# Optimization experiments

Hardware: AMD Instinct MI355X
Metric: run time of the kernel (lower is better)

Reference implementation:

```python
import jax, jax.numpy as jnp
import numpy as np

B, D, C = 4096, 4096, 1024


def setup_inputs() -> dict:
    key = jax.random.key(0)
    kx, kw = jax.random.split(key)
    x = jax.random.normal(kx, (B, D), dtype=jnp.float32)
    # kaiming_normal_ with nonlinearity='relu': std = sqrt(2 / fan_in)
    W = jax.random.normal(kw, (C, D), dtype=jnp.float32) * jnp.sqrt(2.0 / D)
    return {"x": x, "W": W}


def reference(x, W):
    # Original: -( (x[:, :, None] - W.T[None, :, :])**2 ).mean(axis=1)
    d = x.shape[1]
    x_sq = jnp.sum(x * x, axis=1, keepdims=True)        # [B, 1]
    w_sq = jnp.sum(W * W, axis=1)[None, :]              # [1, C]
    cross = jnp.einsum('bd,cd->bc', x, W)               # [B, C] tensor-core GEMM
    return -(x_sq - 2.0 * cross + w_sq) / d
```

## Files before the change

kernel.cpp:

```cpp
#include <hip/hip_runtime.h>
#include <hip/hip_bf16.h>


typedef float f32x4 __attribute__((ext_vector_type(4)));
typedef float f32x2 __attribute__((ext_vector_type(2)));
typedef float f32x16 __attribute__((ext_vector_type(16)));
typedef int i32x4 __attribute__((ext_vector_type(4)));
typedef int i32x8 __attribute__((ext_vector_type(8)));

#define BDIM 4096
#define DDIM 4096
#define CDIM 1024
#define TM 128
#define TN 128
#define BK 64
#define KSPLIT 4
#define NIT ((DDIM / KSPLIT) / BK)
#define SCALE 32.0f
#define INV_SS (1.0f/1024.0f)
#define PSCALE 0.0625f

#define WAITV(N) asm volatile("s_waitcnt vmcnt(" #N ")" ::: "memory")

__global__ __launch_bounds__(256) void cvt_rowsq(
    const float* __restrict__ x, const float* __restrict__ W,
    unsigned char* __restrict__ xb, unsigned char* __restrict__ wb,
    float* __restrict__ xsq, float* __restrict__ wsq)
{
    const int lane = threadIdx.x & 63;
    const int row = blockIdx.x * 4 + (threadIdx.x >> 6);

    const float* src;
    unsigned char* dst;
    float* sq;
    if (row < BDIM) {
        src = x + (size_t)row * DDIM;
        dst = xb + (size_t)row * DDIM;
        sq = xsq + row;
    } else {
        int r = row - BDIM;
        src = W + (size_t)r * DDIM;
        dst = wb + (size_t)r * DDIM;
        sq = wsq + r;
    }

    const float4* s4 = (const float4*)src;
    unsigned int* d4 = (unsigned int*)dst;
    float a = 0.f;
    #pragma unroll
    for (int s = 0; s < DDIM / 4 / 64; ++s) {
        float4 f = s4[lane + 64 * s];
        a += f.x * f.x + f.y * f.y + f.z * f.z + f.w * f.w;
        unsigned int p = 0;
        p = __builtin_amdgcn_cvt_pk_fp8_f32(f.x * SCALE, f.y * SCALE, p, false);
        p = __builtin_amdgcn_cvt_pk_fp8_f32(f.z * SCALE, f.w * SCALE, p, true);
        d4[lane + 64 * s] = p;
    }
    #pragma unroll
    for (int off = 32; off > 0; off >>= 1) a += __shfl_down(a, off);
    if (lane == 0) *sq = a;
}


__device__ __forceinline__ i32x8 cat8(i32x4 lo, i32x4 hi) {
    return __builtin_shufflevector(lo, hi, 0, 1, 2, 3, 4, 5, 6, 7);
}

#define MXMFMA(A, Bv, C)                                                  \
    __builtin_amdgcn_mfma_scale_f32_32x32x64_f8f6f4(                      \
        (A), (Bv), (C), 0, 0, 0, 0x7F7F7F7F, 0, 0x7F7F7F7F)

#define GLOAD16(gp, lp)                                                   \
    __builtin_amdgcn_global_load_lds(                                     \
        (const __attribute__((address_space(1))) void*)(gp),              \
        (__attribute__((address_space(3))) void*)(lp), 16, 0, 0)

__global__ __launch_bounds__(256, 3) void gemm_eucl(
    const unsigned char* __restrict__ xb,
    const unsigned char* __restrict__ wb,
    unsigned int* __restrict__ part)
{
    __shared__ unsigned char sm[3 * 16384];

    const int tid = threadIdx.x;
    const int lane = tid & 63;
    const int w = tid >> 6;
    const int wr = w >> 1;
    const int wc = w & 1;
    const int bm = blockIdx.x * TM;
    const int bn = blockIdx.y * TN;
    const int ks = blockIdx.z * (DDIM / KSPLIT);

    const int srow = w * 32 + (lane >> 2);
    const int schunk = ((lane & 3) ^ ((lane >> 3) & 3)) * 16;
    const unsigned char* gA0 = xb + (size_t)(bm + srow) * DDIM + ks + schunk;
    const unsigned char* gA1 = gA0 + (size_t)16 * DDIM;
    const unsigned char* gB0 = wb + (size_t)(bn + srow) * DDIM + ks + schunk;
    const unsigned char* gB1 = gB0 + (size_t)16 * DDIM;
    unsigned char* lA0 = sm + w * 2048;
    unsigned char* lA1 = lA0 + 1024;
    unsigned char* lB0 = sm + 8192 + w * 2048;
    unsigned char* lB1 = lB0 + 1024;

#define STAGE(q, t)                                                       \
    do {                                                                  \
        GLOAD16(gA0 + (t) * BK, lA0 + (q) * 16384);                       \
        GLOAD16(gA1 + (t) * BK, lA1 + (q) * 16384);                       \
        GLOAD16(gB0 + (t) * BK, lB0 + (q) * 16384);                       \
        GLOAD16(gB1 + (t) * BK, lB1 + (q) * 16384);                       \
    } while (0)

    const int s_rd = ((lane & 31) >> 1) & 3;
    const int c0s = ((lane >> 5) * 2) ^ s_rd;
    const unsigned char* aR0 = sm + (wr * 64 + (lane & 31)) * 64 + c0s * 16;
    const unsigned char* aR1 = sm + (wr * 64 + (lane & 31)) * 64 + (c0s ^ 1) * 16;
    const unsigned char* bR0 = sm + 8192 + (wc * 64 + (lane & 31)) * 64 + c0s * 16;
    const unsigned char* bR1 = sm + 8192 + (wc * 64 + (lane & 31)) * 64 + (c0s ^ 1) * 16;

    f32x16 acc[4] = {};

    STAGE(0, 0);
    STAGE(1, 1);

    #pragma unroll
    for (int t = 0; t < NIT; ++t) {
        const int qo = (t % 3) * 16384;
        if (t + 1 < NIT) WAITV(4);
        else             WAITV(0);
        __builtin_amdgcn_s_barrier();
        if (t + 2 < NIT) STAGE((t + 2) % 3, t + 2);
        i32x8 fb0 = cat8(*(const i32x4*)(bR0 + qo), *(const i32x4*)(bR1 + qo));
        i32x8 fb1 = cat8(*(const i32x4*)(bR0 + qo + 2048),
                         *(const i32x4*)(bR1 + qo + 2048));
        i32x8 fa0 = cat8(*(const i32x4*)(aR0 + qo), *(const i32x4*)(aR1 + qo));
        i32x8 fa1 = cat8(*(const i32x4*)(aR0 + qo + 2048),
                         *(const i32x4*)(aR1 + qo + 2048));
        __builtin_amdgcn_s_setprio(1);
        acc[0] = MXMFMA(fa0, fb0, acc[0]);
        acc[1] = MXMFMA(fa0, fb1, acc[1]);
        acc[2] = MXMFMA(fa1, fb0, acc[2]);
        acc[3] = MXMFMA(fa1, fb1, acc[3]);
        __builtin_amdgcn_s_setprio(0);
    }

    const int bb = blockIdx.x * 8 + blockIdx.y;
    unsigned int* p = part + ((size_t)blockIdx.z * 256 + bb) * 4096;
    #pragma unroll
    for (int f = 0; f < 4; ++f)
        #pragma unroll
        for (int g = 0; g < 4; ++g) {
            unsigned int pk = 0;
            pk = __builtin_amdgcn_cvt_pk_fp8_f32(
                acc[f][g * 4 + 0] * PSCALE, acc[f][g * 4 + 1] * PSCALE, pk, false);
            pk = __builtin_amdgcn_cvt_pk_fp8_f32(
                acc[f][g * 4 + 2] * PSCALE, acc[f][g * 4 + 3] * PSCALE, pk, true);
            p[(f * 4 + g) * 256 + tid] = pk;
        }
#undef STAGE
}

__global__ __launch_bounds__(256) void reduce_out(
    const unsigned int* __restrict__ part, const float* __restrict__ xsq,
    const float* __restrict__ wsq, float* __restrict__ out)
{
    const int bid = blockIdx.x;
    const int bb = bid >> 1;
    const int half = bid & 1;
    const int t = threadIdx.x;
    const int lane = t & 63;
    const int w = t >> 6;
    const int wr = w >> 1, wc = w & 1;
    const int bm = (bb >> 3) * TM, bn = (bb & 7) * TN;
    const size_t sl = (size_t)256 * 4096;
    const float c1 = 2.0f * 16.0f * INV_SS / (float)DDIM;
    const float c2 = 1.0f / (float)DDIM;

    #pragma unroll
    for (int ff = 0; ff < 8; ++ff) {
        const int fg = half * 8 + ff;
        const int f = fg >> 2;
        const int g = fg & 3;
        size_t o = ((size_t)bb * 16 + fg) * 256 + t;
        f32x2 s01 = {0.f, 0.f}, s23 = {0.f, 0.f};
        #pragma unroll
        for (int z = 0; z < KSPLIT; ++z) {
            unsigned int u = part[o + (size_t)z * sl];
            s01 += __builtin_amdgcn_cvt_pk_f32_fp8(u, false);
            s23 += __builtin_amdgcn_cvt_pk_f32_fp8(u, true);
        }
        const int i = f >> 1, j = f & 1;
        const int gn = bn + wc * 64 + j * 32 + (lane & 31);
        const float wv = wsq[gn];
        const int gm0 = bm + wr * 64 + i * 32 + g * 8 + (lane >> 5) * 4;
        float sv[4] = {s01.x, s01.y, s23.x, s23.y};
        #pragma unroll
        for (int r = 0; r < 4; ++r) {
            out[(size_t)(gm0 + r) * CDIM + gn] = sv[r] * c1 - (xsq[gm0 + r] + wv) * c2;
        }
    }
}

__global__ void fallback_kernel(const float* __restrict__ x, const float* __restrict__ W,
                                float* __restrict__ out)
{
    int c = blockIdx.x * blockDim.x + threadIdx.x;
    int b = blockIdx.y;
    if (c >= CDIM) return;
    const float* xr = x + (size_t)b * DDIM;
    const float* wr = W + (size_t)c * DDIM;
    float xs = 0.f, ws = 0.f, cr = 0.f;
    for (int d = 0; d < DDIM; ++d) {
        float xv = xr[d], wv = wr[d];
        xs += xv * xv; ws += wv * wv; cr += xv * wv;
    }
    out[(size_t)b * CDIM + c] = (2.0f * cr - xs - ws) / (float)DDIM;
}

extern "C" void kernel_launch(void* const* d_in, const int* in_sizes, int n_in,
                              void* d_out, int out_size, void* d_ws, size_t ws_size,
                              hipStream_t stream) {
    const float* x = (const float*)d_in[0];
    const float* W = (const float*)d_in[1];
    float* out = (float*)d_out;

    size_t need = (size_t)(BDIM + CDIM) * DDIM
                + (size_t)(BDIM + CDIM) * sizeof(float)
                + (size_t)KSPLIT * BDIM * CDIM;
    if (ws_size < need) {
        fallback_kernel<<<dim3(CDIM / 256, BDIM), 256, 0, stream>>>(x, W, out);
        return;
    }

    unsigned char* xb = (unsigned char*)d_ws;
    unsigned char* wb = xb + (size_t)BDIM * DDIM;
    float* xsq = (float*)(wb + (size_t)CDIM * DDIM);
    float* wsq = xsq + BDIM;
    unsigned int* part = (unsigned int*)(wsq + CDIM);

    cvt_rowsq<<<(BDIM + CDIM) / 4, 256, 0, stream>>>(x, W, xb, wb, xsq, wsq);
    gemm_eucl<<<dim3(BDIM / TM, CDIM / TN, KSPLIT), 256, 0, stream>>>(xb, wb, part);
    reduce_out<<<512, 256, 0, stream>>>(part, xsq, wsq, out);
}
```

Measured before the change: 139.8 us.

## Drop split-K and fuse epilogue into GEMM kernel with 4-stage LDS ring

Removes the K-split of the FP8 GEMM, so each block walks the full reduction and writes the final distance output directly. This eliminates the quantized partial buffer and the separate reduce kernel launch. The LDS ring grows from 3 to 4 stages with an unrolled main loop and peeled tail. Only 256 blocks now run, which may underfill the 256 CUs and lengthen each block, in exchange for less memory traffic and one fewer launch.

```diff
diff --git a/kernel.cpp b/kernel.cpp
--- a/kernel.cpp
+++ b/kernel.cpp
@@ -14,13 +14,12 @@
 #define TM 128
 #define TN 128
 #define BK 64
-#define KSPLIT 4
-#define NIT ((DDIM / KSPLIT) / BK)
+#define NIT (DDIM / BK)
 #define SCALE 32.0f
 #define INV_SS (1.0f/1024.0f)
-#define PSCALE 0.0625f
 
 #define WAITV(N) asm volatile("s_waitcnt vmcnt(" #N ")" ::: "memory")
+#define BAR()    __builtin_amdgcn_s_barrier()
 
 __global__ __launch_bounds__(256) void cvt_rowsq(
     const float* __restrict__ x, const float* __restrict__ W,
@@ -75,12 +74,13 @@
         (const __attribute__((address_space(1))) void*)(gp),              \
         (__attribute__((address_space(3))) void*)(lp), 16, 0, 0)
 
-__global__ __launch_bounds__(256, 3) void gemm_eucl(
+__global__ __launch_bounds__(256) void gemm_eucl(
     const unsigned char* __restrict__ xb,
     const unsigned char* __restrict__ wb,
-    unsigned int* __restrict__ part)
+    const float* __restrict__ xsq, const float* __restrict__ wsq,
+    float* __restrict__ out)
 {
-    __shared__ unsigned char sm[3 * 16384];
+    __shared__ unsigned char sm[4 * 16384];
 
     const int tid = threadIdx.x;
     const int lane = tid & 63;
@@ -89,13 +89,12 @@
     const int wc = w & 1;
     const int bm = blockIdx.x * TM;
     const int bn = blockIdx.y * TN;
-    const int ks = blockIdx.z * (DDIM / KSPLIT);
 
     const int srow = w * 32 + (lane >> 2);
     const int schunk = ((lane & 3) ^ ((lane >> 3) & 3)) * 16;
-    const unsigned char* gA0 = xb + (size_t)(bm + srow) * DDIM + ks + schunk;
+    const unsigned char* gA0 = xb + (size_t)(bm + srow) * DDIM + schunk;
     const unsigned char* gA1 = gA0 + (size_t)16 * DDIM;
-    const unsigned char* gB0 = wb + (size_t)(bn + srow) * DDIM + ks + schunk;
+    const unsigned char* gB0 = wb + (size_t)(bn + srow) * DDIM + schunk;
     const unsigned char* gB1 = gB0 + (size_t)16 * DDIM;
     unsigned char* lA0 = sm + w * 2048;
     unsigned char* lA1 = lA0 + 1024;
@@ -119,85 +118,58 @@
 
     f32x16 acc[4] = {};
 
+#define COMPUTE(qo)                                                       \
+    do {                                                                  \
+        i32x8 fb0 = cat8(*(const i32x4*)(bR0 + (qo)),                     \
+                         *(const i32x4*)(bR1 + (qo)));                    \
+        i32x8 fb1 = cat8(*(const i32x4*)(bR0 + (qo) + 2048),              \
+                         *(const i32x4*)(bR1 + (qo) + 2048));             \
+        i32x8 fa0 = cat8(*(const i32x4*)(aR0 + (qo)),                     \
+                         *(const i32x4*)(aR1 + (qo)));                    \
+        i32x8 fa1 = cat8(*(const i32x4*)(aR0 + (qo) + 2048),              \
+                         *(const i32x4*)(aR1 + (qo) + 2048));             \
+        __builtin_amdgcn_s_setprio(1);                                    \
+        acc[0] = MXMFMA(fa0, fb0, acc[0]);                                \
+        acc[1] = MXMFMA(fa0, fb1, acc[1]);                                \
+        acc[2] = MXMFMA(fa1, fb0, acc[2]);                                \
+        acc[3] = MXMFMA(fa1, fb1, acc[3]);                                \
+        __builtin_amdgcn_s_setprio(0);                                    \
+    } while (0)
+
     STAGE(0, 0);
     STAGE(1, 1);
 
+    #pragma unroll 4
+    for (int t = 0; t < NIT - 2; ++t) {
+        WAITV(4);
+        BAR();
+        STAGE((t + 2) & 3, t + 2);
+        COMPUTE((t & 3) * 16384);
+    }
+    WAITV(4); BAR(); COMPUTE(((NIT - 2) & 3) * 16384);
+    WAITV(0); BAR(); COMPUTE(((NIT - 1) & 3) * 16384);
+
+    const float c1m = 2.0f * INV_SS / (float)DDIM;
+    const float c2 = 1.0f / (float)DDIM;
+    const int gn0 = bn + wc * 64 + (lane & 31);
+    const int gm_b = bm + wr * 64 + (lane >> 5) * 4;
+    const float wv0 = wsq[gn0];
+    const float wv1 = wsq[gn0 + 32];
     #pragma unroll
-    for (int t = 0; t < NIT; ++t) {
-        const int qo = (t % 3) * 16384;
-        if (t + 1 < NIT) WAITV(4);
-        else             WAITV(0);
-        __builtin_amdgcn_s_barrier();
-        if (t + 2 < NIT) STAGE((t + 2) % 3, t + 2);
-        i32x8 fb0 = cat8(*(const i32x4*)(bR0 + qo), *(const i32x4*)(bR1 + qo));
-        i32x8 fb1 = cat8(*(const i32x4*)(bR0 + qo + 2048),
-                         *(const i32x4*)(bR1 + qo + 2048));
-        i32x8 fa0 = cat8(*(const i32x4*)(aR0 + qo), *(const i32x4*)(aR1 + qo));
-        i32x8 fa1 = cat8(*(const i32x4*)(aR0 + qo + 2048),
-                         *(const i32x4*)(aR1 + qo + 2048));
-        __builtin_amdgcn_s_setprio(1);
-        acc[0] = MXMFMA(fa0, fb0, acc[0]);
-        acc[1] = MXMFMA(fa0, fb1, acc[1]);
-        acc[2] = MXMFMA(fa1, fb0, acc[2]);
-        acc[3] = MXMFMA(fa1, fb1, acc[3]);
-        __builtin_amdgcn_s_setprio(0);
-    }
-
-    const int bb = blockIdx.x * 8 + blockIdx.y;
-    unsigned int* p = part + ((size_t)blockIdx.z * 256 + bb) * 4096;
-    #pragma unroll
-    for (int f = 0; f < 4; ++f)
+    for (int i = 0; i < 2; ++i)
         #pragma unroll
-        for (int g = 0; g < 4; ++g) {
-            unsigned int pk = 0;
-            pk = __builtin_amdgcn_cvt_pk_fp8_f32(
-                acc[f][g * 4 + 0] * PSCALE, acc[f][g * 4 + 1] * PSCALE, pk, false);
-            pk = __builtin_amdgcn_cvt_pk_fp8_f32(
-                acc[f][g * 4 + 2] * PSCALE, acc[f][g * 4 + 3] * PSCALE, pk, true);
-            p[(f * 4 + g) * 256 + tid] = pk;
-        }
+        for (int g = 0; g < 4; ++g)
+            #pragma unroll
+            for (int r = 0; r < 4; ++r) {
+                const int gm = gm_b + i * 32 + g * 8 + r;
+                const float xs = xsq[gm];
+                out[(size_t)gm * CDIM + gn0] =
+                    acc[i * 2 + 0][g * 4 + r] * c1m - (xs + wv0) * c2;
+                out[(size_t)gm * CDIM + gn0 + 32] =
+                    acc[i * 2 + 1][g * 4 + r] * c1m - (xs + wv1) * c2;
+            }
 #undef STAGE
-}
-
-__global__ __launch_bounds__(256) void reduce_out(
-    const unsigned int* __restrict__ part, const float* __restrict__ xsq,
-    const float* __restrict__ wsq, float* __restrict__ out)
-{
-    const int bid = blockIdx.x;
-    const int bb = bid >> 1;
-    const int half = bid & 1;
-    const int t = threadIdx.x;
-    const int lane = t & 63;
-    const int w = t >> 6;
-    const int wr = w >> 1, wc = w & 1;
-    const int bm = (bb >> 3) * TM, bn = (bb & 7) * TN;
-    const size_t sl = (size_t)256 * 4096;
-    const float c1 = 2.0f * 16.0f * INV_SS / (float)DDIM;
-    const float c2 = 1.0f / (float)DDIM;
-
-    #pragma unroll
-    for (int ff = 0; ff < 8; ++ff) {
-        const int fg = half * 8 + ff;
-        const int f = fg >> 2;
-        const int g = fg & 3;
-        size_t o = ((size_t)bb * 16 + fg) * 256 + t;
-        f32x2 s01 = {0.f, 0.f}, s23 = {0.f, 0.f};
-        #pragma unroll
-        for (int z = 0; z < KSPLIT; ++z) {
-            unsigned int u = part[o + (size_t)z * sl];
-            s01 += __builtin_amdgcn_cvt_pk_f32_fp8(u, false);
-            s23 += __builtin_amdgcn_cvt_pk_f32_fp8(u, true);
-        }
-        const int i = f >> 1, j = f & 1;
-        const int gn = bn + wc * 64 + j * 32 + (lane & 31);
-        const float wv = wsq[gn];
-        const int gm0 = bm + wr * 64 + i * 32 + g * 8 + (lane >> 5) * 4;
-        float sv[4] = {s01.x, s01.y, s23.x, s23.y};
-        #pragma unroll
-        for (int r = 0; r < 4; ++r) {
-            out[(size_t)(gm0 + r) * CDIM + gn] = sv[r] * c1 - (xsq[gm0 + r] + wv) * c2;
-        }
-    }
+#undef COMPUTE
 }
 
 __global__ void fallback_kernel(const float* __restrict__ x, const float* __restrict__ W,
@@ -224,8 +196,7 @@
     float* out = (float*)d_out;
 
     size_t need = (size_t)(BDIM + CDIM) * DDIM
-                + (size_t)(BDIM + CDIM) * sizeof(float)
-                + (size_t)KSPLIT * BDIM * CDIM;
+                + (size_t)(BDIM + CDIM) * sizeof(float);
     if (ws_size < need) {
         fallback_kernel<<<dim3(CDIM / 256, BDIM), 256, 0, stream>>>(x, W, out);
         return;
@@ -235,9 +206,7 @@
     unsigned char* wb = xb + (size_t)BDIM * DDIM;
     float* xsq = (float*)(wb + (size_t)CDIM * DDIM);
     float* wsq = xsq + BDIM;
-    unsigned int* part = (unsigned int*)(wsq + CDIM);
 
     cvt_rowsq<<<(BDIM + CDIM) / 4, 256, 0, stream>>>(x, W, xb, wb, xsq, wsq);
-    gemm_eucl<<<dim3(BDIM / TM, CDIM / TN, KSPLIT), 256, 0, stream>>>(xb, wb, part);
-    reduce_out<<<512, 256, 0, stream>>>(part, xsq, wsq, out);
-}
+    gemm_eucl<<<dim3(BDIM / TM, CDIM / TN), 256, 0, stream>>>(xb, wb, xsq, wsq, out);
+}
```

New measurement: 132.5 us, median of 2. 5.2% less time.
